# Performance work log

Hardware: AMD Instinct MI355X
Metric: run time of the kernel (lower is better)

## Reference

```python
import jax, jax.numpy as jnp
import numpy as np
import math

_OFFSETS = sorted(set(range(0, 33)) | {48, 64, 96, 128, 192, 256, 384, 512, 768, 1024, 1536})
B, N, D, H, FFN = 1, 2048, 1024, 16, 2816
EPS = 1e-6


def _rmsnorm(x, scale):
    rms = jnp.sqrt(jnp.mean(x * x, axis=-1, keepdims=True) + EPS)
    return scale * (x / rms)


def setup_inputs() -> dict:
    key = jax.random.key(0)
    ks = jax.random.split(key, 8)
    s = 0.02
    alphas = jnp.linspace(0.2, 2.0, H)
    delta_vals = jnp.array([math.log(1.0 + max(d, 0.2)) for d in _OFFSETS], dtype=jnp.float32)
    pos_bias = -delta_vals[:, None] * alphas[None, :]  # (n_offsets, H)
    return {
        "x": jax.random.normal(ks[0], (B, N, D), jnp.float32),
        "norm1_scale": jnp.ones((D,), jnp.float32),
        "norm2_scale": jnp.ones((D,), jnp.float32),
        "w_qkv": jax.random.normal(ks[1], (D, 3 * D), jnp.float32) * s,
        "w_out": jax.random.normal(ks[2], (D, D), jnp.float32) * s,
        "w_gate": jax.random.normal(ks[3], (D, D), jnp.float32) * s,
        "b_gate": jnp.full((D,), 2.0, jnp.float32),
        "pos_bias": pos_bias,
        "w_ffn_gate": jax.random.normal(ks[4], (D, FFN), jnp.float32) * s,
        "w_ffn_up": jax.random.normal(ks[5], (D, FFN), jnp.float32) * s,
        "w_ffn_down": jax.random.normal(ks[6], (FFN, D), jnp.float32) * s,
        "offsets": jnp.array(_OFFSETS, dtype=jnp.int32),
    }


def reference(x, norm1_scale, norm2_scale, w_qkv, w_out, w_gate, b_gate,
              pos_bias, w_ffn_gate, w_ffn_up, w_ffn_down, offsets):
    Bx, Nx, Dx = x.shape
    HD = Dx // H
    # --- attention branch: x + attn(norm1(x)) ---
    xn = _rmsnorm(x, norm1_scale)
    qkv = xn @ w_qkv
    q, k, v = jnp.split(qkv, 3, axis=-1)
    to_heads = lambda t: t.reshape(Bx, Nx, H, HD).transpose(0, 2, 1, 3)  # (B,H,N,HD)
    q, k, v = to_heads(q), to_heads(k), to_heads(v)

    t_idx = jnp.arange(Nx)
    # gather positions t-delta per (query t, offset o); clamped positions are masked below
    src = jnp.clip(t_idx[:, None] - offsets[None, :], 0, None)  # (N, O)
    Kg = k[:, :, src, :]  # (B,H,N,O,HD)
    Vg = v[:, :, src, :]

    scale = HD ** (-0.5)
    scores = jnp.einsum('bhnd,bhnod->bhno', q, Kg) * scale
    scores = scores + pos_bias.T[None, :, None, :]  # (1,H,1,O)
    invalid = t_idx[:, None] < offsets[None, :]      # (N, O)
    scores = jnp.where(invalid[None, None], -jnp.inf, scores)
    alpha = jax.nn.softmax(scores, axis=-1)
    out = jnp.einsum('bhno,bhnod->bhnd', alpha, Vg)
    out = out.transpose(0, 2, 1, 3).reshape(Bx, Nx, Dx)

    gate = jax.nn.sigmoid(xn @ w_gate + b_gate)
    x = x + (out * gate) @ w_out

    # --- FFN branch: x + SwiGLU(norm2(x)) ---
    xn2 = _rmsnorm(x, norm2_scale)
    x = x + (jax.nn.silu(xn2 @ w_ffn_gate) * (xn2 @ w_ffn_up)) @ w_ffn_down
    return x
```

## Files before the change

### kernel.cpp

```cpp
#include <hip/hip_runtime.h>
#include <hip/hip_bf16.h>
#include <math.h>

typedef __bf16 bf16;
typedef __bf16 v8bf __attribute__((ext_vector_type(8)));
typedef __bf16 v4bf __attribute__((ext_vector_type(4)));
typedef float v4f __attribute__((ext_vector_type(4)));

#define N_TOK 2048
#define DIM 1024
#define NH 16
#define FFN_DIM 2816

#define GLL(g, l) __builtin_amdgcn_global_load_lds(                         \
    (const __attribute__((address_space(1))) uint32_t*)(g),                 \
    (__attribute__((address_space(3))) uint32_t*)(l), 16, 0, 0)

#define WAITV(n) do {                                                        \
    switch (n) {                                                             \
    case 0: asm volatile("s_waitcnt vmcnt(0)" ::: "memory"); break;          \
    case 2: asm volatile("s_waitcnt vmcnt(2)" ::: "memory"); break;          \
    case 3: asm volatile("s_waitcnt vmcnt(3)" ::: "memory"); break;          \
    case 4: asm volatile("s_waitcnt vmcnt(4)" ::: "memory"); break;          \
    case 6: asm volatile("s_waitcnt vmcnt(6)" ::: "memory"); break;          \
    case 8: asm volatile("s_waitcnt vmcnt(8)" ::: "memory"); break;          \
    case 9: asm volatile("s_waitcnt vmcnt(9)" ::: "memory"); break;          \
    default: asm volatile("s_waitcnt vmcnt(0)" ::: "memory"); break; }       \
} while (0)

__global__ __launch_bounds__(256) void transpose_all_kernel(
    const float* __restrict__ w_qkv, const float* __restrict__ w_gate,
    const float* __restrict__ w_out, const float* __restrict__ w_ffng,
    const float* __restrict__ w_ffnu, const float* __restrict__ w_ffnd,
    bf16* __restrict__ wqkvgT, bf16* __restrict__ woutT,
    bf16* __restrict__ wcatT, bf16* __restrict__ wffndT)
{
    int bid = blockIdx.x;
    const float* W; bf16* D; int Kd, Nc, nb, kb, dstbase;
    if (bid < 3072) {
        W = w_qkv; D = wqkvgT; Kd = 1024; Nc = 3072;
        nb = (bid % 96) * 32; kb = (bid / 96) * 32; dstbase = nb;
    } else if (bid < 4096) { int b = bid - 3072;
        W = w_gate; D = wqkvgT; Kd = 1024; Nc = 1024;
        nb = (b % 32) * 32; kb = (b / 32) * 32; dstbase = 3072 + nb;
    } else if (bid < 5120) { int b = bid - 4096;
        W = w_out; D = woutT; Kd = 1024; Nc = 1024;
        nb = (b % 32) * 32; kb = (b / 32) * 32; dstbase = nb;
    } else if (bid < 7936) { int b = bid - 5120;
        W = w_ffng; D = wcatT; Kd = 1024; Nc = 2816;
        nb = (b % 88) * 32; kb = (b / 88) * 32;
        dstbase = (nb >> 6) * 128 + (nb & 63);
    } else if (bid < 10752) { int b = bid - 7936;
        W = w_ffnu; D = wcatT; Kd = 1024; Nc = 2816;
        nb = (b % 88) * 32; kb = (b / 88) * 32;
        dstbase = (nb >> 6) * 128 + 64 + (nb & 63);
    } else { int b = bid - 10752;
        W = w_ffnd; D = wffndT; Kd = 2816; Nc = 1024;
        nb = (b % 32) * 32; kb = (b / 32) * 32; dstbase = nb;
    }
    __shared__ float tile[32][33];
    int tx = threadIdx.x, ty = threadIdx.y;
#pragma unroll
    for (int r = 0; r < 4; ++r)
        tile[ty + r * 8][tx] = W[(size_t)(kb + ty + r * 8) * Nc + nb + tx];
    __syncthreads();
#pragma unroll
    for (int r = 0; r < 4; ++r)
        D[(size_t)(dstbase + ty + r * 8) * Kd + kb + tx] = (bf16)tile[tx][ty + r * 8];
}

__global__ __launch_bounds__(256) void rmsnorm_kernel(
    const float* __restrict__ x, const float* __restrict__ scale, bf16* __restrict__ out)
{
    int row = blockIdx.x, tid = threadIdx.x;
    float4 v = ((const float4*)(x + (size_t)row * DIM))[tid];
    float ss = v.x * v.x + v.y * v.y + v.z * v.z + v.w * v.w;
#pragma unroll
    for (int off = 32; off > 0; off >>= 1) ss += __shfl_down(ss, off);
    __shared__ float ps[4];
    if ((tid & 63) == 0) ps[tid >> 6] = ss;
    __syncthreads();
    float tot = ps[0] + ps[1] + ps[2] + ps[3];
    float inv = rsqrtf(tot * (1.0f / DIM) + 1e-6f);
    float4 s = ((const float4*)scale)[tid];
    union { bf16 b[4]; uint2 u; } p;
    p.b[0] = (bf16)(v.x * inv * s.x);
    p.b[1] = (bf16)(v.y * inv * s.y);
    p.b[2] = (bf16)(v.z * inv * s.z);
    p.b[3] = (bf16)(v.w * inv * s.w);
    ((uint2*)(out + (size_t)row * DIM))[tid] = p.u;
}

__global__ __launch_bounds__(256) void attn_kernel(
    const bf16* __restrict__ qkvg, const int* __restrict__ offs,
    const float* __restrict__ pos_bias, bf16* __restrict__ attgb)
{
    constexpr int O = 44;
    const int t = blockIdx.x, tid = threadIdx.x;
    const int wv = tid >> 6, lane = tid & 63;
    const int h1 = lane >> 2, l4 = lane & 3;
    const size_t RS = 4 * DIM;
    __shared__ float sS[O][17];
    __shared__ float sPB[O * 16];
    __shared__ int so[O];
    __shared__ float sAcc[4 * 1024];
    if (tid < O) so[tid] = offs[tid];
    for (int i = tid; i < O * 16; i += 256) sPB[i] = pos_bias[i];
    __syncthreads();

    const bf16* qbase = qkvg + (size_t)t * RS + h1 * 64;
    v8bf q0v = *(const v8bf*)(qbase + l4 * 8);
    v8bf q1v = *(const v8bf*)(qbase + 32 + l4 * 8);
    float qa[16];
#pragma unroll
    for (int e = 0; e < 8; ++e) {
        qa[e] = (float)q0v[e] * 0.125f;
        qa[8 + e] = (float)q1v[e] * 0.125f;
    }

#pragma unroll 4
    for (int it = 0; it < 11; ++it) {
        const int o = it * 4 + wv;
        const int src = t - so[o];
        const int srcc = src < 0 ? 0 : src;
        const bf16* kbase = qkvg + (size_t)srcc * RS + DIM + h1 * 64;
        v8bf k0 = *(const v8bf*)(kbase + l4 * 8);
        v8bf k1 = *(const v8bf*)(kbase + 32 + l4 * 8);
        float p = 0.f;
#pragma unroll
        for (int e = 0; e < 8; ++e) p += qa[e] * (float)k0[e];
#pragma unroll
        for (int e = 0; e < 8; ++e) p += qa[8 + e] * (float)k1[e];
        p += __shfl_xor(p, 1);
        p += __shfl_xor(p, 2);
        float s = (src >= 0) ? p + sPB[o * NH + h1] : -INFINITY;
        if (l4 == 0) sS[o][h1] = s;
    }
    __syncthreads();

    const int h = tid >> 4, j16 = tid & 15;
    float mx = -INFINITY;
#pragma unroll
    for (int o = j16; o < O; o += 16) mx = fmaxf(mx, sS[o][h]);
    mx = fmaxf(mx, __shfl_xor(mx, 1));
    mx = fmaxf(mx, __shfl_xor(mx, 2));
    mx = fmaxf(mx, __shfl_xor(mx, 4));
    mx = fmaxf(mx, __shfl_xor(mx, 8));
    float sum = 0.f;
#pragma unroll
    for (int o = j16; o < O; o += 16) {
        float e = __expf(sS[o][h] - mx);
        sS[o][h] = e;
        sum += e;
    }
    sum += __shfl_xor(sum, 1);
    sum += __shfl_xor(sum, 2);
    sum += __shfl_xor(sum, 4);
    sum += __shfl_xor(sum, 8);
    float inv = 1.0f / sum;
    __syncthreads();

    const int h2 = lane >> 2;
    const int dbase = lane * 16;
    float pacc[16] = {};
#pragma unroll 4
    for (int it = 0; it < 11; ++it) {
        int o = it * 4 + wv;
        int src = t - so[o];
        int srcc = src < 0 ? 0 : src;
        float a = sS[o][h2];
        const bf16* vb = qkvg + (size_t)srcc * RS + 2 * DIM + dbase;
        v8bf v0 = *(const v8bf*)(vb);
        v8bf v1 = *(const v8bf*)(vb + 8);
#pragma unroll
        for (int e = 0; e < 8; ++e) {
            pacc[e] += a * (float)v0[e];
            pacc[8 + e] += a * (float)v1[e];
        }
    }
#pragma unroll
    for (int q = 0; q < 4; ++q) {
        int phys = lane * 4 + (q ^ (lane & 3));
        *(float4*)&sAcc[wv * 1024 + phys * 4] =
            make_float4(pacc[q * 4], pacc[q * 4 + 1], pacc[q * 4 + 2], pacc[q * 4 + 3]);
    }
    __syncthreads();

    const int lr = tid >> 2, qr = tid & 3;
    const int phys = lr * 4 + (qr ^ (lr & 3));
    float4 p0 = *(const float4*)&sAcc[0 * 1024 + phys * 4];
    float4 p1 = *(const float4*)&sAcc[1 * 1024 + phys * 4];
    float4 p2 = *(const float4*)&sAcc[2 * 1024 + phys * 4];
    float4 p3 = *(const float4*)&sAcc[3 * 1024 + phys * 4];
    v4bf gv = *(const v4bf*)(qkvg + (size_t)t * RS + 3 * DIM + tid * 4);
    v4bf ov;
    ov[0] = (bf16)((p0.x + p1.x + p2.x + p3.x) * inv * (float)gv[0]);
    ov[1] = (bf16)((p0.y + p1.y + p2.y + p3.y) * inv * (float)gv[1]);
    ov[2] = (bf16)((p0.z + p1.z + p2.z + p3.z) * inv * (float)gv[2]);
    ov[3] = (bf16)((p0.w + p1.w + p2.w + p3.w) * inv * (float)gv[3]);
    *(v4bf*)(attgb + (size_t)t * DIM + tid * 4) = ov;
}

template<int BM, int BN, int NTHR, int NBUF, int EPI>
__global__ __launch_bounds__(NTHR) void gemm_kernel(
    const bf16* __restrict__ A, const bf16* __restrict__ Bt,
    int M, int N, int K,
    float* __restrict__ outf, bf16* __restrict__ outb,
    const float* __restrict__ e1, const float* __restrict__ bias)
{
    constexpr int WAVES = NTHR / 64;
    constexpr int WCOLS = WAVES / 2;
    constexpr int WME = BM / 2;
    constexpr int WNE = BN / WCOLS;
    constexpr int MI = WME / 16;
    constexpr int NJ = WNE / 16;
    constexpr int CH_A = BM * 4, CH_B = BN * 4;
    constexpr int LPT = (CH_A + CH_B) / NTHR;
    constexpr int STAGE_BYTES = NBUF * (BM + BN) * 32 * 2;
    constexpr int EPI_BYTES = (EPI == 6) ? BM * 66 * 4 : 0;
    constexpr int SMEM_BYTES = STAGE_BYTES > EPI_BYTES ? STAGE_BYTES : EPI_BYTES;
    __shared__ __align__(16) char smem[SMEM_BYTES];
    bf16* AsB = (bf16*)smem;
    bf16* BsB = (bf16*)(smem + NBUF * BM * 32 * 2);

    const int tid = threadIdx.x;
    const int m0 = blockIdx.y * BM, n0 = blockIdx.x * BN;
    const int lane = tid & 63, wave = tid >> 6;
    const int wr = wave / WCOLS, wc = wave % WCOLS;
    const int wm = wr * WME, wn = wc * WNE;
    const int lrow = lane & 15, l16 = lane >> 4;

    const bf16* gptr[LPT];
    int lo[LPT];
    bool pa[LPT];
#pragma unroll
    for (int i = 0; i < LPT; ++i) {
        int c = tid + i * NTHR;
        bool inA = c < CH_A;
        int cc = inA ? c : c - CH_A;
        int r = cc >> 2, q = cc & 3;
        int gq = (q ^ ((r >> 1) & 3)) * 8;
        gptr[i] = inA ? A + (size_t)(m0 + r) * K + gq
                      : Bt + (size_t)(n0 + r) * K + gq;
        lo[i] = r * 32 + q * 8;
        pa[i] = inA;
    }

    auto STAGE = [&](int b, int kt) {
        const int ko = kt * 32;
#pragma unroll
        for (int i = 0; i < LPT; ++i) {
            bf16* dst = (pa[i] ? AsB + b * BM * 32 : BsB + b * BN * 32) + lo[i];
            GLL(gptr[i] + ko, dst);
        }
    };

    v4f acc[MI][NJ] = {};
    auto COMPUTE = [&](int b) {
        v8bf af[MI], bfr[NJ];
#pragma unroll
        for (int i = 0; i < MI; ++i) {
            int r = wm + i * 16 + lrow;
            af[i] = *(v8bf*)&AsB[b * BM * 32 + r * 32 + ((l16 ^ ((r >> 1) & 3)) * 8)];
        }
#pragma unroll
        for (int j = 0; j < NJ; ++j) {
            int r = wn + j * 16 + lrow;
            bfr[j] = *(v8bf*)&BsB[b * BN * 32 + r * 32 + ((l16 ^ ((r >> 1) & 3)) * 8)];
        }
        __builtin_amdgcn_s_setprio(1);
#pragma unroll
        for (int i = 0; i < MI; ++i)
#pragma unroll
            for (int j = 0; j < NJ; ++j)
                acc[i][j] = __builtin_amdgcn_mfma_f32_16x16x32_bf16(af[i], bfr[j], acc[i][j], 0, 0, 0);
        __builtin_amdgcn_s_setprio(0);
    };

    const int NT = K >> 5;
#pragma unroll
    for (int i = 0; i < NBUF; ++i) STAGE(i, i);
    for (int t = 0; t < NT - (NBUF - 1); ++t) {
        WAITV((NBUF - 1) * LPT);
        __builtin_amdgcn_s_barrier();
        __builtin_amdgcn_sched_barrier(0);
        COMPUTE(t & (NBUF - 1));
        __builtin_amdgcn_sched_barrier(0);
        __builtin_amdgcn_s_barrier();
        if (t + NBUF < NT) STAGE(t & (NBUF - 1), t + NBUF);
    }
#pragma unroll
    for (int e = NBUF - 1; e >= 1; --e) {
        const int t = NT - e;
        WAITV((e - 1) * LPT);
        __builtin_amdgcn_s_barrier();
        __builtin_amdgcn_sched_barrier(0);
        COMPUTE(t & (NBUF - 1));
        __builtin_amdgcn_sched_barrier(0);
        __builtin_amdgcn_s_barrier();
    }

    if constexpr (EPI == 6) {
        float* eps = (float*)smem;
        const bool isGate = (wn < 64);
        if (isGate) {
#pragma unroll
            for (int i = 0; i < MI; ++i)
#pragma unroll
                for (int j = 0; j < NJ; ++j)
#pragma unroll
                    for (int r = 0; r < 4; ++r) {
                        int rowL = wm + i * 16 + l16 * 4 + r;
                        int colL = wn + j * 16 + lrow;
                        eps[rowL * 66 + colL] = acc[i][j][r];
                    }
        }
        asm volatile("s_waitcnt lgkmcnt(0)" ::: "memory");
        __builtin_amdgcn_s_barrier();
        if (!isGate) {
            const int halfN = N >> 1;
#pragma unroll
            for (int i = 0; i < MI; ++i)
#pragma unroll
                for (int j = 0; j < NJ; ++j)
#pragma unroll
                    for (int r = 0; r < 4; ++r) {
                        int rowL = wm + i * 16 + l16 * 4 + r;
                        int colU = wn - 64 + j * 16 + lrow;
                        float g = eps[rowL * 66 + colU];
                        float sil = g / (1.0f + __expf(-g));
                        float u = acc[i][j][r];
                        outb[(size_t)(m0 + rowL) * halfN + (n0 >> 1) + colU] = (bf16)(sil * u);
                    }
        }
        return;
    }

#pragma unroll
    for (int i = 0; i < MI; ++i)
#pragma unroll
        for (int j = 0; j < NJ; ++j)
#pragma unroll
            for (int r = 0; r < 4; ++r) {
                int row = m0 + wm + i * 16 + l16 * 4 + r;
                int col = n0 + wn + j * 16 + lrow;
                size_t idx = (size_t)row * N + col;
                float v = acc[i][j][r];
                if constexpr (EPI == 3) {
                    outf[idx] = e1[idx] + v;
                } else if constexpr (EPI == 5) {
                    if (col >= 3 * DIM) {
                        float g = 1.0f / (1.0f + __expf(-(v + bias[col - 3 * DIM])));
                        outb[idx] = (bf16)g;
                    } else {
                        outb[idx] = (bf16)v;
                    }
                }
            }
}

extern "C" void kernel_launch(void* const* d_in, const int* in_sizes, int n_in,
                              void* d_out, int out_size, void* d_ws, size_t ws_size,
                              hipStream_t stream)
{
    const float* x        = (const float*)d_in[0];
    const float* n1s      = (const float*)d_in[1];
    const float* n2s      = (const float*)d_in[2];
    const float* w_qkv    = (const float*)d_in[3];
    const float* w_out    = (const float*)d_in[4];
    const float* w_gate   = (const float*)d_in[5];
    const float* b_gate   = (const float*)d_in[6];
    const float* pos_bias = (const float*)d_in[7];
    const float* w_ffng   = (const float*)d_in[8];
    const float* w_ffnu   = (const float*)d_in[9];
    const float* w_ffnd   = (const float*)d_in[10];
    const int* offsets    = (const int*)d_in[11];
    float* out = (float*)d_out;

    char* ws = (char*)d_ws;
    size_t cur = 0;
    auto alloc = [&](size_t bytes) -> void* {
        void* p = ws + cur;
        cur += (bytes + 255) & ~(size_t)255;
        return p;
    };
    bf16*  xnb    = (bf16*)alloc((size_t)N_TOK * DIM * 2);
    bf16*  qkvgb  = (bf16*)alloc((size_t)N_TOK * 4 * DIM * 2);
    bf16*  attgb  = (bf16*)alloc((size_t)N_TOK * DIM * 2);
    float* x1     = (float*)alloc((size_t)N_TOK * DIM * 4);
    bf16*  xn2b   = (bf16*)alloc((size_t)N_TOK * DIM * 2);
    bf16*  hb     = (bf16*)alloc((size_t)N_TOK * FFN_DIM * 2);
    bf16*  wqkvgT = (bf16*)alloc((size_t)4 * DIM * DIM * 2);
    bf16*  woutT  = (bf16*)alloc((size_t)DIM * DIM * 2);
    bf16*  wcatT  = (bf16*)alloc((size_t)2 * FFN_DIM * DIM * 2);
    bf16*  wffndT = (bf16*)alloc((size_t)FFN_DIM * DIM * 2);

    transpose_all_kernel<<<13568, dim3(32, 8), 0, stream>>>(
        w_qkv, w_gate, w_out, w_ffng, w_ffnu, w_ffnd,
        wqkvgT, woutT, wcatT, wffndT);

    rmsnorm_kernel<<<N_TOK, 256, 0, stream>>>(x, n1s, xnb);
    gemm_kernel<64, 128, 256, 2, 5><<<dim3(32, 32), 256, 0, stream>>>(
        xnb, wqkvgT, N_TOK, 4 * DIM, DIM, nullptr, qkvgb, nullptr, b_gate);
    attn_kernel<<<dim3(N_TOK), 256, 0, stream>>>(qkvgb, offsets, pos_bias, attgb);
    gemm_kernel<64, 64, 256, 4, 3><<<dim3(16, 32), 256, 0, stream>>>(
        attgb, woutT, N_TOK, DIM, DIM, x1, nullptr, x, nullptr);
    rmsnorm_kernel<<<N_TOK, 256, 0, stream>>>(x1, n2s, xn2b);
    gemm_kernel<64, 128, 256, 2, 6><<<dim3(44, 32), 256, 0, stream>>>(
        xn2b, wcatT, N_TOK, 2 * FFN_DIM, DIM, nullptr, hb, nullptr, nullptr);
    gemm_kernel<64, 64, 256, 4, 3><<<dim3(16, 32), 256, 0, stream>>>(
        hb, wffndT, N_TOK, DIM, FFN_DIM, out, nullptr, x1, nullptr);
}
```

Measured before the change: 167.0 us.

## Use 128x128 tiles, XCD-aware block swizzle, and 3-stage pipeline for big GEMMs

Adds an optional block-index remap that gives each XCD a contiguous range of tiles, walking down M first, so neighbouring tiles share operands in the per-XCD L2. The QKV+gate and FFN gate/up GEMMs move to 128x128 tiles with 512 threads and three buffers. The pipeline indexing changes from bitmasks to modulo so a non-power-of-two buffer count works. Larger tiles raise operand reuse but cut the number of blocks and may lower occupancy. The EPI 6 epilogue, which assumed a 64-row tile, now runs with BM=128.

```diff
diff --git a/kernel.cpp b/kernel.cpp
--- a/kernel.cpp
+++ b/kernel.cpp
@@ -201,7 +201,7 @@
     *(v4bf*)(attgb + (size_t)t * DIM + tid * 4) = ov;
 }
 
-template<int BM, int BN, int NTHR, int NBUF, int EPI>
+template<int BM, int BN, int NTHR, int NBUF, int EPI, int SWZ>
 __global__ __launch_bounds__(NTHR) void gemm_kernel(
     const bf16* __restrict__ A, const bf16* __restrict__ Bt,
     int M, int N, int K,
@@ -224,7 +224,19 @@
     bf16* BsB = (bf16*)(smem + NBUF * BM * 32 * 2);
 
     const int tid = threadIdx.x;
-    const int m0 = blockIdx.y * BM, n0 = blockIdx.x * BN;
+    int m0, n0;
+    if constexpr (SWZ) {
+        const int nx = gridDim.x, ny = gridDim.y;
+        const int w = blockIdx.y * nx + blockIdx.x;
+        const int total = nx * ny, q = total >> 3, r = total & 7;
+        const int xcd = w & 7, i = w >> 3;
+        const int f = xcd * q + (xcd < r ? xcd : r) + i;
+        m0 = (f % ny) * BM;
+        n0 = (f / ny) * BN;
+    } else {
+        m0 = blockIdx.y * BM;
+        n0 = blockIdx.x * BN;
+    }
     const int lane = tid & 63, wave = tid >> 6;
     const int wr = wave / WCOLS, wc = wave % WCOLS;
     const int wm = wr * WME, wn = wc * WNE;
@@ -278,24 +290,25 @@
     };
 
     const int NT = K >> 5;
-#pragma unroll
-    for (int i = 0; i < NBUF; ++i) STAGE(i, i);
-    for (int t = 0; t < NT - (NBUF - 1); ++t) {
-        WAITV((NBUF - 1) * LPT);
+    constexpr int PIPE = NBUF >= 3 ? NBUF : NBUF;
+#pragma unroll
+    for (int i = 0; i < PIPE; ++i) STAGE(i % NBUF, i);
+    for (int t = 0; t < NT - (PIPE - 1); ++t) {
+        WAITV((PIPE - 1) * LPT);
         __builtin_amdgcn_s_barrier();
         __builtin_amdgcn_sched_barrier(0);
-        COMPUTE(t & (NBUF - 1));
+        COMPUTE(t % NBUF);
         __builtin_amdgcn_sched_barrier(0);
         __builtin_amdgcn_s_barrier();
-        if (t + NBUF < NT) STAGE(t & (NBUF - 1), t + NBUF);
-    }
-#pragma unroll
-    for (int e = NBUF - 1; e >= 1; --e) {
+        if (t + PIPE < NT) STAGE(t % NBUF, t + PIPE);
+    }
+#pragma unroll
+    for (int e = PIPE - 1; e >= 1; --e) {
         const int t = NT - e;
         WAITV((e - 1) * LPT);
         __builtin_amdgcn_s_barrier();
         __builtin_amdgcn_sched_barrier(0);
-        COMPUTE(t & (NBUF - 1));
+        COMPUTE(t % NBUF);
         __builtin_amdgcn_sched_barrier(0);
         __builtin_amdgcn_s_barrier();
     }
@@ -400,14 +413,14 @@
         wqkvgT, woutT, wcatT, wffndT);
 
     rmsnorm_kernel<<<N_TOK, 256, 0, stream>>>(x, n1s, xnb);
-    gemm_kernel<64, 128, 256, 2, 5><<<dim3(32, 32), 256, 0, stream>>>(
+    gemm_kernel<128, 128, 512, 3, 5, 1><<<dim3(32, 16), 512, 0, stream>>>(
         xnb, wqkvgT, N_TOK, 4 * DIM, DIM, nullptr, qkvgb, nullptr, b_gate);
     attn_kernel<<<dim3(N_TOK), 256, 0, stream>>>(qkvgb, offsets, pos_bias, attgb);
-    gemm_kernel<64, 64, 256, 4, 3><<<dim3(16, 32), 256, 0, stream>>>(
+    gemm_kernel<64, 64, 256, 4, 3, 0><<<dim3(16, 32), 256, 0, stream>>>(
         attgb, woutT, N_TOK, DIM, DIM, x1, nullptr, x, nullptr);
     rmsnorm_kernel<<<N_TOK, 256, 0, stream>>>(x1, n2s, xn2b);
-    gemm_kernel<64, 128, 256, 2, 6><<<dim3(44, 32), 256, 0, stream>>>(
+    gemm_kernel<128, 128, 512, 3, 6, 1><<<dim3(44, 16), 512, 0, stream>>>(
         xn2b, wcatT, N_TOK, 2 * FFN_DIM, DIM, nullptr, hb, nullptr, nullptr);
-    gemm_kernel<64, 64, 256, 4, 3><<<dim3(16, 32), 256, 0, stream>>>(
+    gemm_kernel<64, 64, 256, 4, 3, 1><<<dim3(16, 32), 256, 0, stream>>>(
         hb, wffndT, N_TOK, DIM, FFN_DIM, out, nullptr, x1, nullptr);
 }
```

Measured after the change: 157.1 us. 6.0% less time.
